# Kernel tuning notes

Measured on AMD Instinct MI355X. Metric: run time of the kernel, lower is better.

## Reference

```python
import jax, jax.numpy as jnp
import numpy as np

C = 512
H = 8
D = C // H
GROUPS = 32
EPS = 1e-5

def setup_inputs() -> dict:
    key = jax.random.key(0)
    ks = jax.random.split(key, 7)
    B, L = 4, 2048
    x = jax.random.normal(ks[0], (B, C, L), dtype=jnp.float32)
    gamma = jnp.ones((C,), dtype=jnp.float32)
    beta = jnp.zeros((C,), dtype=jnp.float32)
    w_qkv = jax.random.normal(ks[1], (3 * C, C), dtype=jnp.float32) * (1.0 / np.sqrt(C))
    b_qkv = jax.random.normal(ks[2], (3 * C,), dtype=jnp.float32) * 0.01
    w_proj = jax.random.normal(ks[3], (C, C), dtype=jnp.float32) * (1.0 / np.sqrt(C))
    b_proj = jax.random.normal(ks[4], (C,), dtype=jnp.float32) * 0.01
    return {"x": x, "gamma": gamma, "beta": beta, "w_qkv": w_qkv,
            "b_qkv": b_qkv, "w_proj": w_proj, "b_proj": b_proj}

def _group_norm(x, gamma, beta):
    B, Cc, L = x.shape
    xg = x.reshape(B, GROUPS, Cc // GROUPS, L)
    mean = jnp.mean(xg, axis=(2, 3), keepdims=True)
    var = jnp.var(xg, axis=(2, 3), keepdims=True)
    xn = ((xg - mean) * jax.lax.rsqrt(var + EPS)).reshape(B, Cc, L)
    return xn * gamma[None, :, None] + beta[None, :, None]

def reference(x, gamma, beta, w_qkv, b_qkv, w_proj, b_proj):
    B, Cc, L = x.shape
    h = _group_norm(x, gamma, beta)
    # 1x1 conv == channel matmul: (3C,C) x (B,C,L) -> (B,3C,L)
    qkv = jnp.einsum('oc,bcl->bol', w_qkv, h) + b_qkv[None, :, None]
    q, k, v = jnp.split(qkv, 3, axis=1)
    # (B,C,L) -> (B,H,L,D)
    def to_heads(t):
        return t.reshape(B, H, D, L).transpose(0, 1, 3, 2)
    q, k, v = to_heads(q), to_heads(k), to_heads(v)
    scale = 1.0 / np.sqrt(D).astype(np.float32)
    attn = jnp.einsum('bhqd,bhkd->bhqk', q, k) * scale  # [B,H,L,L]
    attn = jax.nn.softmax(attn, axis=-1)
    out = jnp.einsum('bhqk,bhkd->bhqd', attn, v)  # [B,H,L,D]
    out = out.transpose(0, 1, 3, 2).reshape(B, Cc, L)
    proj = jnp.einsum('oc,bcl->bol', w_proj, out) + b_proj[None, :, None]
    return x + proj
```

## Files before the change

kernel.cpp:

```cpp
#include <hip/hip_runtime.h>
#include <stdint.h>

#define C_DIM 512
#define H_HEADS 8
#define D_HEAD 64
#define B_BATCH 4
#define L_SEQ 2048
#define GROUPS 32
#define EPS_GN 1e-5f

typedef unsigned short u16;
typedef __attribute__((ext_vector_type(8))) __bf16 bf16x8;
typedef __attribute__((ext_vector_type(2))) float f32x2;
typedef __attribute__((ext_vector_type(4))) float f32x4;
typedef __attribute__((ext_vector_type(16))) float f32x16;

__device__ __forceinline__ u16 f2bf(float f) {
  unsigned u = __builtin_bit_cast(unsigned, f);
  unsigned r = u + 0x7FFFu + ((u >> 16) & 1u);
  return (u16)(r >> 16);
}

__device__ __forceinline__ unsigned cvtpk_bf16(float lo, float hi) {
  unsigned r;
  asm("v_cvt_pk_bf16_f32 %0, %1, %2" : "=v"(r) : "v"(lo), "v"(hi));
  return r;
}

__device__ __forceinline__ void pl32swap(unsigned& a, unsigned& b) {
  asm("v_permlane32_swap_b32 %0, %1" : "+v"(a), "+v"(b));
}

__device__ __forceinline__ bf16x8 mk8(unsigned a, unsigned b, unsigned c, unsigned d) {
  union { uint4 u; bf16x8 v; } z;
  z.u.x = a; z.u.y = b; z.u.z = c; z.u.w = d;
  return z.v;
}

__device__ __forceinline__ void gl16(const void* g, void* l) {
  __builtin_amdgcn_global_load_lds((const __attribute__((address_space(1))) void*)g,
                                   (__attribute__((address_space(3))) void*)l, 16, 0, 0);
}

__global__ __launch_bounds__(256) void prep_kernel(const float* __restrict__ x,
                                                   const float* __restrict__ gamma,
                                                   const float* __restrict__ beta,
                                                   const float* __restrict__ wq,
                                                   const float* __restrict__ wp,
                                                   u16* __restrict__ h_t,
                                                   u16* __restrict__ wq_bf,
                                                   u16* __restrict__ wp_bf) {
  if (blockIdx.x >= 128) {
    int i = (blockIdx.x - 128) * 256 + threadIdx.x;
    const int nq = 3 * C_DIM * C_DIM;
    int idx = i * 4;
    const float* src;
    u16* dst;
    if (idx < nq) { src = wq + idx; dst = wq_bf + idx; }
    else          { src = wp + (idx - nq); dst = wp_bf + (idx - nq); }
    float4 v = *(const float4*)src;
    uint2 pk;
    pk.x = cvtpk_bf16(v.x, v.y);
    pk.y = cvtpk_bf16(v.z, v.w);
    *(uint2*)dst = pk;
    return;
  }
  int bg = blockIdx.x;
  int b = bg >> 5, g = bg & 31;
  const float* base = x + ((size_t)(b * C_DIM + g * 16)) * L_SEQ;
  int t = threadIdx.x;
  int w = t >> 6;
  float s = 0.f, sq = 0.f;
  for (int i = 0; i < 32; ++i) {
    float4 v = ((const float4*)base)[t + i * 256];
    s += v.x + v.y + v.z + v.w;
    sq += v.x * v.x + v.y * v.y + v.z * v.z + v.w * v.w;
  }
  for (int off = 32; off; off >>= 1) { s += __shfl_down(s, off); sq += __shfl_down(sq, off); }
  __shared__ float red[8];
  if ((t & 63) == 0) { red[w * 2] = s; red[w * 2 + 1] = sq; }
  __syncthreads();
  float ts = red[0] + red[2] + red[4] + red[6];
  float tq = red[1] + red[3] + red[5] + red[7];
  float mean = ts * (1.f / 32768.f);
  float var = tq * (1.f / 32768.f) - mean * mean;
  float rstd = rsqrtf(var + EPS_GN);
  float ga[16], be[16];
#pragma unroll
  for (int c = 0; c < 16; ++c) {
    float gm = gamma[g * 16 + c];
    ga[c] = gm * rstd;
    be[c] = beta[g * 16 + c] - mean * gm * rstd;
  }
  __shared__ float tile[16][260];
  for (int lc = 0; lc < 8; ++lc) {
    __syncthreads();
#pragma unroll
    for (int it = 0; it < 4; ++it) {
      int r = it * 4 + w;
      int c4 = (t & 63) * 4;
      *(float4*)&tile[r][c4] = *(const float4*)(base + (size_t)r * L_SEQ + lc * 256 + c4);
    }
    __syncthreads();
    int l = lc * 256 + t;
    unsigned wds[8];
#pragma unroll
    for (int c = 0; c < 8; ++c) {
      float a0 = tile[2 * c][t] * ga[2 * c] + be[2 * c];
      float a1 = tile[2 * c + 1][t] * ga[2 * c + 1] + be[2 * c + 1];
      wds[c] = cvtpk_bf16(a0, a1);
    }
    u16* dst = h_t + ((size_t)(b * L_SEQ + l)) * C_DIM + g * 16;
    uint4 p0; p0.x = wds[0]; p0.y = wds[1]; p0.z = wds[2]; p0.w = wds[3];
    uint4 p1; p1.x = wds[4]; p1.y = wds[5]; p1.z = wds[6]; p1.w = wds[7];
    *(uint4*)dst = p0;
    *(uint4*)(dst + 8) = p1;
  }
}

template <int MODE>
__global__ __launch_bounds__(256) void gemm_kernel(const u16* __restrict__ A_bf,
                                                   const u16* __restrict__ B_t,
                                                   const float* __restrict__ bias,
                                                   const float* __restrict__ xres,
                                                   u16* __restrict__ q_t,
                                                   u16* __restrict__ kf_g,
                                                   u16* __restrict__ vf_g,
                                                   float* __restrict__ out_f) {
  constexpr int K = 512;
  __shared__ u16 A_lds[128][32];
  __shared__ u16 B_lds[128][32];
  int t = threadIdx.x;
  int w = t >> 6, lane = t & 63;
  int q4 = lane >> 4, c15 = lane & 15;
  int wm = w >> 1, wn = w & 1;
  int o0 = blockIdx.y * 128;
  int l0 = blockIdx.x * 128;
  int b = blockIdx.z;
  const u16* Bb = B_t + (size_t)b * L_SEQ * K;
  f32x4 acc[4][4] = {};

  int sr = lane >> 2, sc = lane & 3;
  int r0 = w * 32 + sr;
  int r1 = r0 + 16;
  int lc0 = (sc - (r0 >> 1)) & 3;
  int lc1 = (sc - (r1 >> 1)) & 3;
  const u16* Ag0 = A_bf + (size_t)(o0 + r0) * K + lc0 * 8;
  const u16* Ag1 = A_bf + (size_t)(o0 + r1) * K + lc1 * 8;
  const u16* Bg0 = Bb + (size_t)(l0 + r0) * K + lc0 * 8;
  const u16* Bg1 = Bb + (size_t)(l0 + r1) * K + lc1 * 8;
  u16* Al0 = &A_lds[w * 32][0];
  u16* Al1 = &A_lds[w * 32 + 16][0];
  u16* Bl0 = &B_lds[w * 32][0];
  u16* Bl1 = &B_lds[w * 32 + 16][0];

  for (int kt = 0; kt < K / 32; ++kt) {
    gl16(Ag0, Al0); gl16(Ag1, Al1);
    gl16(Bg0, Bl0); gl16(Bg1, Bl1);
    Ag0 += 32; Ag1 += 32; Bg0 += 32; Bg1 += 32;
    __syncthreads();
    bf16x8 af[4], bfr[4];
#pragma unroll
    for (int mi = 0; mi < 4; ++mi) {
      int ar = wm * 64 + mi * 16 + c15;
      af[mi] = *(const bf16x8*)&A_lds[ar][((q4 + (ar >> 1)) & 3) * 8];
    }
#pragma unroll
    for (int ni = 0; ni < 4; ++ni) {
      int br = wn * 64 + ni * 16 + c15;
      bfr[ni] = *(const bf16x8*)&B_lds[br][((q4 + (br >> 1)) & 3) * 8];
    }
#pragma unroll
    for (int mi = 0; mi < 4; ++mi)
#pragma unroll
      for (int ni = 0; ni < 4; ++ni)
        acc[mi][ni] = __builtin_amdgcn_mfma_f32_16x16x32_bf16(af[mi], bfr[ni], acc[mi][ni], 0, 0, 0);
    __syncthreads();
  }

  if (MODE == 0) {
    const float QS = 0.18033688f;
    int sel = o0 >> 9;
    int ob = o0 - sel * 512 + wm * 64;
#pragma unroll
    for (int mi = 0; mi < 4; ++mi) {
      int orow = ob + mi * 16 + q4 * 4;
      float4 bi = *(const float4*)&bias[o0 + wm * 64 + mi * 16 + q4 * 4];
#pragma unroll
      for (int ni = 0; ni < 4; ++ni) {
        int l = l0 + wn * 64 + ni * 16 + c15;
        float v0 = acc[mi][ni][0] + bi.x;
        float v1 = acc[mi][ni][1] + bi.y;
        float v2 = acc[mi][ni][2] + bi.z;
        float v3 = acc[mi][ni][3] + bi.w;
        if (sel == 0) {
          v0 *= QS; v1 *= QS; v2 *= QS; v3 *= QS;
          uint2 pk;
          pk.x = cvtpk_bf16(v0, v1);
          pk.y = cvtpk_bf16(v2, v3);
          *(uint2*)(q_t + ((size_t)(b * L_SEQ + l)) * C_DIM + orow) = pk;
        } else if (sel == 1) {
          int hh = orow >> 6, d = orow & 63;
          size_t base = ((size_t)(b * 8 + hh)) * 131072 +
                        (size_t)(((l >> 5) * 4 + (d >> 4))) * 512 +
                        (size_t)((l & 31) + ((d >> 3) & 1) * 32) * 8 + (d & 7);
          uint2 pk;
          pk.x = cvtpk_bf16(v0, v1);
          pk.y = cvtpk_bf16(v2, v3);
          *(uint2*)(kf_g + base) = pk;
        } else {
          int hh = orow >> 6, d = orow & 63;
          size_t base0 = ((size_t)(b * 8 + hh)) * 131072 +
                         (size_t)(l >> 4) * 1024 +
                         (size_t)((l >> 3) & 1) * 256 + (l & 7);
          vf_g[base0 + (size_t)((d + 0) >> 5) * 512 + ((d + 0) & 31) * 8] = f2bf(v0);
          vf_g[base0 + (size_t)((d + 1) >> 5) * 512 + ((d + 1) & 31) * 8] = f2bf(v1);
          vf_g[base0 + (size_t)((d + 2) >> 5) * 512 + ((d + 2) & 31) * 8] = f2bf(v2);
          vf_g[base0 + (size_t)((d + 3) >> 5) * 512 + ((d + 3) & 31) * 8] = f2bf(v3);
        }
      }
    }
  } else {
#pragma unroll
    for (int mi = 0; mi < 4; ++mi) {
      int orow = o0 + wm * 64 + mi * 16 + q4 * 4;
      float4 bi = *(const float4*)&bias[orow];
#pragma unroll
      for (int ni = 0; ni < 4; ++ni) {
        int l = l0 + wn * 64 + ni * 16 + c15;
        size_t base2 = ((size_t)(b * C_DIM + orow)) * L_SEQ + l;
        out_f[base2] = acc[mi][ni][0] + bi.x + xres[base2];
        out_f[base2 + L_SEQ] = acc[mi][ni][1] + bi.y + xres[base2 + L_SEQ];
        out_f[base2 + 2 * L_SEQ] = acc[mi][ni][2] + bi.z + xres[base2 + 2 * L_SEQ];
        out_f[base2 + 3 * L_SEQ] = acc[mi][ni][3] + bi.w + xres[base2 + 3 * L_SEQ];
      }
    }
  }
}

#define ATILE(KC, KN, T)                                                       \
  {                                                                            \
    int tn = (T) + 1; tn = tn > 31 ? 31 : tn;                                  \
    const u16* kp = kfb + tn * 2048;                                           \
    const u16* vp = vfb + (T) * 2048;                                          \
    KN[0] = *(const bf16x8*)(kp);                                              \
    KN[1] = *(const bf16x8*)(kp + 512);                                        \
    KN[2] = *(const bf16x8*)(kp + 1024);                                       \
    KN[3] = *(const bf16x8*)(kp + 1536);                                       \
    bf16x8 v0 = *(const bf16x8*)(vp);                                          \
    bf16x8 v1 = *(const bf16x8*)(vp + 512);                                    \
    bf16x8 v2 = *(const bf16x8*)(vp + 1024);                                   \
    bf16x8 v3 = *(const bf16x8*)(vp + 1536);                                   \
    f32x16 s;                                                                  \
    _Pragma("unroll") for (int r = 0; r < 16; ++r) s[r] = 0.f;                 \
    s = __builtin_amdgcn_mfma_f32_32x32x16_bf16(KC[0], qf[0], s, 0, 0, 0);     \
    s = __builtin_amdgcn_mfma_f32_32x32x16_bf16(KC[1], qf[1], s, 0, 0, 0);     \
    s = __builtin_amdgcn_mfma_f32_32x32x16_bf16(KC[2], qf[2], s, 0, 0, 0);     \
    s = __builtin_amdgcn_mfma_f32_32x32x16_bf16(KC[3], qf[3], s, 0, 0, 0);     \
    f32x2 p0_ = {s[0], s[1]}, p1_ = {s[2], s[3]}, p2_ = {s[4], s[5]},          \
          p3_ = {s[6], s[7]}, p4_ = {s[8], s[9]}, p5_ = {s[10], s[11]},        \
          p6_ = {s[12], s[13]}, p7_ = {s[14], s[15]};                          \
    f32x2 M0 = __builtin_elementwise_max(__builtin_elementwise_max(p0_, p1_),  \
                                         __builtin_elementwise_max(p2_, p3_)); \
    f32x2 M1 = __builtin_elementwise_max(__builtin_elementwise_max(p4_, p5_),  \
                                         __builtin_elementwise_max(p6_, p7_)); \
    f32x2 M = __builtin_elementwise_max(M0, M1);                               \
    float mx = fmaxf(M[0], M[1]);                                              \
    mx = fmaxf(mx, __shfl_xor(mx, 32));                                        \
    if (__any(mx > m_r + 8.f)) {                                               \
      float mnew = fmaxf(m_r, mx);                                             \
      float al = __builtin_amdgcn_exp2f(m_r - mnew);                           \
      l_r *= al;                                                               \
      _Pragma("unroll") for (int r = 0; r < 16; ++r) { o0[r] *= al; o1[r] *= al; } \
      m_r = mnew;                                                              \
    }                                                                          \
    _Pragma("unroll") for (int r = 0; r < 16; ++r)                             \
        s[r] = __builtin_amdgcn_exp2f(s[r] - m_r);                             \
    f32x2 a0_ = {s[0], s[1]}, a1_ = {s[2], s[3]}, a2_ = {s[4], s[5]},          \
          a3_ = {s[6], s[7]}, a4_ = {s[8], s[9]}, a5_ = {s[10], s[11]},        \
          a6_ = {s[12], s[13]}, a7_ = {s[14], s[15]};                          \
    f32x2 b0_ = a0_ + a1_, b1_ = a2_ + a3_, b2_ = a4_ + a5_, b3_ = a6_ + a7_;  \
    f32x2 c0_ = b0_ + b1_, c1_ = b2_ + b3_;                                    \
    f32x2 d0_ = c0_ + c1_;                                                     \
    float sum = d0_[0] + d0_[1];                                               \
    sum += __shfl_xor(sum, 32);                                                \
    l_r += sum;                                                                \
    unsigned pk[8];                                                            \
    _Pragma("unroll") for (int i = 0; i < 8; ++i)                              \
        pk[i] = cvtpk_bf16(s[2 * i], s[2 * i + 1]);                            \
    pl32swap(pk[0], pk[2]); pl32swap(pk[1], pk[3]);                            \
    pl32swap(pk[4], pk[6]); pl32swap(pk[5], pk[7]);                            \
    bf16x8 pf0 = mk8(pk[0], pk[1], pk[2], pk[3]);                              \
    bf16x8 pf1 = mk8(pk[4], pk[5], pk[6], pk[7]);                              \
    o0 = __builtin_amdgcn_mfma_f32_32x32x16_bf16(v0, pf0, o0, 0, 0, 0);        \
    o1 = __builtin_amdgcn_mfma_f32_32x32x16_bf16(v1, pf0, o1, 0, 0, 0);        \
    o0 = __builtin_amdgcn_mfma_f32_32x32x16_bf16(v2, pf1, o0, 0, 0, 0);        \
    o1 = __builtin_amdgcn_mfma_f32_32x32x16_bf16(v3, pf1, o1, 0, 0, 0);        \
  }

__global__ __launch_bounds__(256, 4) void attn_kernel(const u16* __restrict__ q_t,
                                                      const u16* __restrict__ kf_g,
                                                      const u16* __restrict__ vf_g,
                                                      u16* __restrict__ ao_t) {
  __shared__ float oL[4][64][32];
  __shared__ float mL[4][32];
  __shared__ float lL[4][32];

  int g = blockIdx.x;
  int wk = (g & 7) * 128 + (g >> 3);
  int qg = wk & 31, bh = wk >> 5;
  int b = bh >> 3, h = bh & 7;
  int t = threadIdx.x;
  int wv = t >> 6, lane = t & 63;
  int q = lane & 31, hi = lane >> 5;
  int qh = wv & 1, kvh = wv >> 1;
  int q0 = qg * 64 + qh * 32;

  const u16* qp = q_t + ((size_t)(b * L_SEQ + q0 + q)) * C_DIM + h * 64 + hi * 8;
  bf16x8 qf[4];
#pragma unroll
  for (int kk = 0; kk < 4; ++kk) qf[kk] = *(const bf16x8*)(qp + kk * 16);

  const u16* kfb = kf_g + (size_t)bh * 131072 + (size_t)kvh * 65536 + lane * 8;
  const u16* vfb = vf_g + (size_t)bh * 131072 + (size_t)kvh * 65536 + lane * 8;

  f32x16 o0, o1;
#pragma unroll
  for (int r = 0; r < 16; ++r) { o0[r] = 0.f; o1[r] = 0.f; }
  float m_r = -1e30f, l_r = 0.f;

  bf16x8 kA[4], kB[4];
#pragma unroll
  for (int i = 0; i < 4; ++i) kA[i] = *(const bf16x8*)(kfb + i * 512);

  for (int it = 0; it < 16; ++it) {
    ATILE(kA, kB, 2 * it);
    ATILE(kB, kA, 2 * it + 1);
  }

  if (hi == 0) mL[wv][q] = m_r;
  __syncthreads();
  float ms = fmaxf(mL[wv][q], mL[wv ^ 2][q]);
  float scl = __builtin_amdgcn_exp2f(m_r - ms);
  if (hi == 0) lL[wv][q] = l_r * scl;
#pragma unroll
  for (int r = 0; r < 16; ++r) {
    int d = (r & 3) + 8 * (r >> 2) + 4 * hi;
    oL[wv][d][q] = o0[r] * scl;
    oL[wv][d + 32][q] = o1[r] * scl;
  }
  __syncthreads();

  int tq = t & 31;
  int oqh = (t >> 5) & 1;
  int d0 = (t >> 6) * 16;
  float lsum = lL[oqh][tq] + lL[oqh + 2][tq];
  float inv = 1.f / lsum;
  float v[16];
#pragma unroll
  for (int i = 0; i < 16; ++i)
    v[i] = (oL[oqh][d0 + i][tq] + oL[oqh + 2][d0 + i][tq]) * inv;
  u16* dst = ao_t + ((size_t)(b * L_SEQ + qg * 64 + oqh * 32 + tq)) * C_DIM + h * 64 + d0;
  uint4 ov0, ov1;
  ov0.x = cvtpk_bf16(v[0], v[1]);
  ov0.y = cvtpk_bf16(v[2], v[3]);
  ov0.z = cvtpk_bf16(v[4], v[5]);
  ov0.w = cvtpk_bf16(v[6], v[7]);
  ov1.x = cvtpk_bf16(v[8], v[9]);
  ov1.y = cvtpk_bf16(v[10], v[11]);
  ov1.z = cvtpk_bf16(v[12], v[13]);
  ov1.w = cvtpk_bf16(v[14], v[15]);
  *(uint4*)dst = ov0;
  *(uint4*)(dst + 8) = ov1;
}

extern "C" void kernel_launch(void* const* d_in, const int* in_sizes, int n_in,
                              void* d_out, int out_size, void* d_ws, size_t ws_size,
                              hipStream_t stream) {
  const float* x = (const float*)d_in[0];
  const float* gamma = (const float*)d_in[1];
  const float* beta = (const float*)d_in[2];
  const float* w_qkv = (const float*)d_in[3];
  const float* b_qkv = (const float*)d_in[4];
  const float* w_proj = (const float*)d_in[5];
  const float* b_proj = (const float*)d_in[6];
  float* out = (float*)d_out;

  u16* wq_bf = (u16*)d_ws;
  u16* wp_bf = wq_bf + 786432;
  u16* h_t = wp_bf + 262144;
  u16* q_t = h_t + 4194304;
  u16* kf_g = q_t + 4194304;
  u16* vf_g = kf_g + 4194304;
  u16* ao_t = vf_g + 4194304;

  prep_kernel<<<dim3(1152), dim3(256), 0, stream>>>(x, gamma, beta, w_qkv, w_proj,
                                                    h_t, wq_bf, wp_bf);
  gemm_kernel<0><<<dim3(16, 12, 4), dim3(256), 0, stream>>>(wq_bf, h_t, b_qkv, nullptr, q_t, kf_g, vf_g, nullptr);
  attn_kernel<<<dim3(1024), dim3(256), 0, stream>>>(q_t, kf_g, vf_g, ao_t);
  gemm_kernel<1><<<dim3(16, 4, 4), dim3(256), 0, stream>>>(wp_bf, ao_t, b_proj, x, nullptr, nullptr, nullptr, out);
}
```

Measured before the change: 105.9 us.

## Compute softmax row sums via MFMA with ones, drop K prefetch, retile proj GEMM

```diff
diff --git a/kernel.cpp b/kernel.cpp
--- a/kernel.cpp
+++ b/kernel.cpp
@@ -118,15 +118,12 @@
   }
 }
 
-template <int MODE>
-__global__ __launch_bounds__(256) void gemm_kernel(const u16* __restrict__ A_bf,
-                                                   const u16* __restrict__ B_t,
-                                                   const float* __restrict__ bias,
-                                                   const float* __restrict__ xres,
-                                                   u16* __restrict__ q_t,
-                                                   u16* __restrict__ kf_g,
-                                                   u16* __restrict__ vf_g,
-                                                   float* __restrict__ out_f) {
+__global__ __launch_bounds__(256) void gemm_qkv(const u16* __restrict__ A_bf,
+                                                const u16* __restrict__ B_t,
+                                                const float* __restrict__ bias,
+                                                u16* __restrict__ q_t,
+                                                u16* __restrict__ kf_g,
+                                                u16* __restrict__ vf_g) {
   constexpr int K = 512;
   __shared__ u16 A_lds[128][32];
   __shared__ u16 B_lds[128][32];
@@ -178,124 +175,176 @@
     __syncthreads();
   }
 
-  if (MODE == 0) {
-    const float QS = 0.18033688f;
-    int sel = o0 >> 9;
-    int ob = o0 - sel * 512 + wm * 64;
+  const float QS = 0.18033688f;
+  int sel = o0 >> 9;
+  int ob = o0 - sel * 512 + wm * 64;
+#pragma unroll
+  for (int mi = 0; mi < 4; ++mi) {
+    int orow = ob + mi * 16 + q4 * 4;
+    float4 bi = *(const float4*)&bias[o0 + wm * 64 + mi * 16 + q4 * 4];
+#pragma unroll
+    for (int ni = 0; ni < 4; ++ni) {
+      int l = l0 + wn * 64 + ni * 16 + c15;
+      float v0 = acc[mi][ni][0] + bi.x;
+      float v1 = acc[mi][ni][1] + bi.y;
+      float v2 = acc[mi][ni][2] + bi.z;
+      float v3 = acc[mi][ni][3] + bi.w;
+      if (sel == 0) {
+        v0 *= QS; v1 *= QS; v2 *= QS; v3 *= QS;
+        uint2 pk;
+        pk.x = cvtpk_bf16(v0, v1);
+        pk.y = cvtpk_bf16(v2, v3);
+        *(uint2*)(q_t + ((size_t)(b * L_SEQ + l)) * C_DIM + orow) = pk;
+      } else if (sel == 1) {
+        int hh = orow >> 6, d = orow & 63;
+        size_t base = ((size_t)(b * 8 + hh)) * 131072 +
+                      (size_t)(((l >> 5) * 4 + (d >> 4))) * 512 +
+                      (size_t)((l & 31) + ((d >> 3) & 1) * 32) * 8 + (d & 7);
+        uint2 pk;
+        pk.x = cvtpk_bf16(v0, v1);
+        pk.y = cvtpk_bf16(v2, v3);
+        *(uint2*)(kf_g + base) = pk;
+      } else {
+        int hh = orow >> 6, d = orow & 63;
+        size_t base0 = ((size_t)(b * 8 + hh)) * 131072 +
+                       (size_t)(l >> 4) * 1024 +
+                       (size_t)((l >> 3) & 1) * 256 + (l & 7);
+        vf_g[base0 + (size_t)((d + 0) >> 5) * 512 + ((d + 0) & 31) * 8] = f2bf(v0);
+        vf_g[base0 + (size_t)((d + 1) >> 5) * 512 + ((d + 1) & 31) * 8] = f2bf(v1);
+        vf_g[base0 + (size_t)((d + 2) >> 5) * 512 + ((d + 2) & 31) * 8] = f2bf(v2);
+        vf_g[base0 + (size_t)((d + 3) >> 5) * 512 + ((d + 3) & 31) * 8] = f2bf(v3);
+      }
+    }
+  }
+}
+
+__global__ __launch_bounds__(256) void gemm_proj(const u16* __restrict__ A_bf,
+                                                 const u16* __restrict__ B_t,
+                                                 const float* __restrict__ bias,
+                                                 const float* __restrict__ xres,
+                                                 float* __restrict__ out_f) {
+  constexpr int K = 512;
+  __shared__ u16 A_lds[64][32];
+  __shared__ u16 B_lds[128][32];
+  int t = threadIdx.x;
+  int w = t >> 6, lane = t & 63;
+  int q4 = lane >> 4, c15 = lane & 15;
+  int o0 = blockIdx.y * 64;
+  int l0 = blockIdx.x * 128;
+  int b = blockIdx.z;
+  const u16* Bb = B_t + (size_t)b * L_SEQ * K;
+  f32x4 acc[4][2] = {};
+
+  int sr = lane >> 2, sc = lane & 3;
+  int ra = w * 16 + sr;
+  int lca = (sc - (ra >> 1)) & 3;
+  const u16* Ag = A_bf + (size_t)(o0 + ra) * K + lca * 8;
+  int rb0 = w * 32 + sr, rb1 = rb0 + 16;
+  int lcb0 = (sc - (rb0 >> 1)) & 3;
+  int lcb1 = (sc - (rb1 >> 1)) & 3;
+  const u16* Bg0 = Bb + (size_t)(l0 + rb0) * K + lcb0 * 8;
+  const u16* Bg1 = Bb + (size_t)(l0 + rb1) * K + lcb1 * 8;
+  u16* Al = &A_lds[w * 16][0];
+  u16* Bl0 = &B_lds[w * 32][0];
+  u16* Bl1 = &B_lds[w * 32 + 16][0];
+
+  for (int kt = 0; kt < K / 32; ++kt) {
+    gl16(Ag, Al);
+    gl16(Bg0, Bl0); gl16(Bg1, Bl1);
+    Ag += 32; Bg0 += 32; Bg1 += 32;
+    __syncthreads();
+    bf16x8 af[4], bfr[2];
 #pragma unroll
     for (int mi = 0; mi < 4; ++mi) {
-      int orow = ob + mi * 16 + q4 * 4;
-      float4 bi = *(const float4*)&bias[o0 + wm * 64 + mi * 16 + q4 * 4];
-#pragma unroll
-      for (int ni = 0; ni < 4; ++ni) {
-        int l = l0 + wn * 64 + ni * 16 + c15;
-        float v0 = acc[mi][ni][0] + bi.x;
-        float v1 = acc[mi][ni][1] + bi.y;
-        float v2 = acc[mi][ni][2] + bi.z;
-        float v3 = acc[mi][ni][3] + bi.w;
-        if (sel == 0) {
-          v0 *= QS; v1 *= QS; v2 *= QS; v3 *= QS;
-          uint2 pk;
-          pk.x = cvtpk_bf16(v0, v1);
-          pk.y = cvtpk_bf16(v2, v3);
-          *(uint2*)(q_t + ((size_t)(b * L_SEQ + l)) * C_DIM + orow) = pk;
-        } else if (sel == 1) {
-          int hh = orow >> 6, d = orow & 63;
-          size_t base = ((size_t)(b * 8 + hh)) * 131072 +
-                        (size_t)(((l >> 5) * 4 + (d >> 4))) * 512 +
-                        (size_t)((l & 31) + ((d >> 3) & 1) * 32) * 8 + (d & 7);
-          uint2 pk;
-          pk.x = cvtpk_bf16(v0, v1);
-          pk.y = cvtpk_bf16(v2, v3);
-          *(uint2*)(kf_g + base) = pk;
-        } else {
-          int hh = orow >> 6, d = orow & 63;
-          size_t base0 = ((size_t)(b * 8 + hh)) * 131072 +
-                         (size_t)(l >> 4) * 1024 +
-                         (size_t)((l >> 3) & 1) * 256 + (l & 7);
-          vf_g[base0 + (size_t)((d + 0) >> 5) * 512 + ((d + 0) & 31) * 8] = f2bf(v0);
-          vf_g[base0 + (size_t)((d + 1) >> 5) * 512 + ((d + 1) & 31) * 8] = f2bf(v1);
-          vf_g[base0 + (size_t)((d + 2) >> 5) * 512 + ((d + 2) & 31) * 8] = f2bf(v2);
-          vf_g[base0 + (size_t)((d + 3) >> 5) * 512 + ((d + 3) & 31) * 8] = f2bf(v3);
-        }
-      }
-    }
-  } else {
-#pragma unroll
-    for (int mi = 0; mi < 4; ++mi) {
-      int orow = o0 + wm * 64 + mi * 16 + q4 * 4;
-      float4 bi = *(const float4*)&bias[orow];
-#pragma unroll
-      for (int ni = 0; ni < 4; ++ni) {
-        int l = l0 + wn * 64 + ni * 16 + c15;
-        size_t base2 = ((size_t)(b * C_DIM + orow)) * L_SEQ + l;
-        out_f[base2] = acc[mi][ni][0] + bi.x + xres[base2];
-        out_f[base2 + L_SEQ] = acc[mi][ni][1] + bi.y + xres[base2 + L_SEQ];
-        out_f[base2 + 2 * L_SEQ] = acc[mi][ni][2] + bi.z + xres[base2 + 2 * L_SEQ];
-        out_f[base2 + 3 * L_SEQ] = acc[mi][ni][3] + bi.w + xres[base2 + 3 * L_SEQ];
-      }
-    }
-  }
-}
-
-#define ATILE(KC, KN, T)                                                       \
+      int ar = mi * 16 + c15;
+      af[mi] = *(const bf16x8*)&A_lds[ar][((q4 + (ar >> 1)) & 3) * 8];
+    }
+#pragma unroll
+    for (int ni = 0; ni < 2; ++ni) {
+      int br = w * 32 + ni * 16 + c15;
+      bfr[ni] = *(const bf16x8*)&B_lds[br][((q4 + (br >> 1)) & 3) * 8];
+    }
+#pragma unroll
+    for (int mi = 0; mi < 4; ++mi)
+#pragma unroll
+      for (int ni = 0; ni < 2; ++ni)
+        acc[mi][ni] = __builtin_amdgcn_mfma_f32_16x16x32_bf16(af[mi], bfr[ni], acc[mi][ni], 0, 0, 0);
+    __syncthreads();
+  }
+
+#pragma unroll
+  for (int mi = 0; mi < 4; ++mi) {
+    int orow = o0 + mi * 16 + q4 * 4;
+    float4 bi = *(const float4*)&bias[orow];
+#pragma unroll
+    for (int ni = 0; ni < 2; ++ni) {
+      int l = l0 + w * 32 + ni * 16 + c15;
+      size_t base2 = ((size_t)(b * C_DIM + orow)) * L_SEQ + l;
+      out_f[base2] = acc[mi][ni][0] + bi.x + xres[base2];
+      out_f[base2 + L_SEQ] = acc[mi][ni][1] + bi.y + xres[base2 + L_SEQ];
+      out_f[base2 + 2 * L_SEQ] = acc[mi][ni][2] + bi.z + xres[base2 + 2 * L_SEQ];
+      out_f[base2 + 3 * L_SEQ] = acc[mi][ni][3] + bi.w + xres[base2 + 3 * L_SEQ];
+    }
+  }
+}
+
+#define ATILE(T)                                                               \
   {                                                                            \
-    int tn = (T) + 1; tn = tn > 31 ? 31 : tn;                                  \
-    const u16* kp = kfb + tn * 2048;                                           \
+    const u16* kp = kfb + (T) * 2048;                                          \
     const u16* vp = vfb + (T) * 2048;                                          \
-    KN[0] = *(const bf16x8*)(kp);                                              \
-    KN[1] = *(const bf16x8*)(kp + 512);                                        \
-    KN[2] = *(const bf16x8*)(kp + 1024);                                       \
-    KN[3] = *(const bf16x8*)(kp + 1536);                                       \
+    bf16x8 k0 = *(const bf16x8*)(kp);                                          \
+    bf16x8 k1 = *(const bf16x8*)(kp + 512);                                    \
+    bf16x8 k2 = *(const bf16x8*)(kp + 1024);                                   \
+    bf16x8 k3 = *(const bf16x8*)(kp + 1536);                                   \
+    f32x16 s;                                                                  \
+    _Pragma("unroll") for (int r = 0; r < 16; ++r) s[r] = 0.f;                 \
+    s = __builtin_amdgcn_mfma_f32_32x32x16_bf16(k0, qf[0], s, 0, 0, 0);        \
+    s = __builtin_amdgcn_mfma_f32_32x32x16_bf16(k1, qf[1], s, 0, 0, 0);        \
+    s = __builtin_amdgcn_mfma_f32_32x32x16_bf16(k2, qf[2], s, 0, 0, 0);        \
+    s = __builtin_amdgcn_mfma_f32_32x32x16_bf16(k3, qf[3], s, 0, 0, 0);        \
     bf16x8 v0 = *(const bf16x8*)(vp);                                          \
     bf16x8 v1 = *(const bf16x8*)(vp + 512);                                    \
     bf16x8 v2 = *(const bf16x8*)(vp + 1024);                                   \
     bf16x8 v3 = *(const bf16x8*)(vp + 1536);                                   \
-    f32x16 s;                                                                  \
-    _Pragma("unroll") for (int r = 0; r < 16; ++r) s[r] = 0.f;                 \
-    s = __builtin_amdgcn_mfma_f32_32x32x16_bf16(KC[0], qf[0], s, 0, 0, 0);     \
-    s = __builtin_amdgcn_mfma_f32_32x32x16_bf16(KC[1], qf[1], s, 0, 0, 0);     \
-    s = __builtin_amdgcn_mfma_f32_32x32x16_bf16(KC[2], qf[2], s, 0, 0, 0);     \
-    s = __builtin_amdgcn_mfma_f32_32x32x16_bf16(KC[3], qf[3], s, 0, 0, 0);     \
-    f32x2 p0_ = {s[0], s[1]}, p1_ = {s[2], s[3]}, p2_ = {s[4], s[5]},          \
-          p3_ = {s[6], s[7]}, p4_ = {s[8], s[9]}, p5_ = {s[10], s[11]},        \
-          p6_ = {s[12], s[13]}, p7_ = {s[14], s[15]};                          \
-    f32x2 M0 = __builtin_elementwise_max(__builtin_elementwise_max(p0_, p1_),  \
-                                         __builtin_elementwise_max(p2_, p3_)); \
-    f32x2 M1 = __builtin_elementwise_max(__builtin_elementwise_max(p4_, p5_),  \
-                                         __builtin_elementwise_max(p6_, p7_)); \
+    f32x2 e0 = {s[0], s[1]}, e1 = {s[2], s[3]}, e2 = {s[4], s[5]},             \
+          e3 = {s[6], s[7]}, e4 = {s[8], s[9]}, e5 = {s[10], s[11]},           \
+          e6 = {s[12], s[13]}, e7 = {s[14], s[15]};                            \
+    f32x2 M0 = __builtin_elementwise_max(__builtin_elementwise_max(e0, e1),    \
+                                         __builtin_elementwise_max(e2, e3));   \
+    f32x2 M1 = __builtin_elementwise_max(__builtin_elementwise_max(e4, e5),    \
+                                         __builtin_elementwise_max(e6, e7));   \
     f32x2 M = __builtin_elementwise_max(M0, M1);                               \
     float mx = fmaxf(M[0], M[1]);                                              \
     mx = fmaxf(mx, __shfl_xor(mx, 32));                                        \
     if (__any(mx > m_r + 8.f)) {                                               \
       float mnew = fmaxf(m_r, mx);                                             \
       float al = __builtin_amdgcn_exp2f(m_r - mnew);                           \
-      l_r *= al;                                                               \
-      _Pragma("unroll") for (int r = 0; r < 16; ++r) { o0[r] *= al; o1[r] *= al; } \
+      lacc[0] *= al;                                                           \
+      _Pragma("unroll") for (int r = 0; r < 16; ++r) { o0a[r] *= al; o1a[r] *= al; } \
       m_r = mnew;                                                              \
     }                                                                          \
-    _Pragma("unroll") for (int r = 0; r < 16; ++r)                             \
-        s[r] = __builtin_amdgcn_exp2f(s[r] - m_r);                             \
-    f32x2 a0_ = {s[0], s[1]}, a1_ = {s[2], s[3]}, a2_ = {s[4], s[5]},          \
-          a3_ = {s[6], s[7]}, a4_ = {s[8], s[9]}, a5_ = {s[10], s[11]},        \
-          a6_ = {s[12], s[13]}, a7_ = {s[14], s[15]};                          \
-    f32x2 b0_ = a0_ + a1_, b1_ = a2_ + a3_, b2_ = a4_ + a5_, b3_ = a6_ + a7_;  \
-    f32x2 c0_ = b0_ + b1_, c1_ = b2_ + b3_;                                    \
-    f32x2 d0_ = c0_ + c1_;                                                     \
-    float sum = d0_[0] + d0_[1];                                               \
-    sum += __shfl_xor(sum, 32);                                                \
-    l_r += sum;                                                                \
+    f32x2 nm = {-m_r, -m_r};                                                   \
+    e0 += nm; e1 += nm; e2 += nm; e3 += nm;                                    \
+    e4 += nm; e5 += nm; e6 += nm; e7 += nm;                                    \
     unsigned pk[8];                                                            \
-    _Pragma("unroll") for (int i = 0; i < 8; ++i)                              \
-        pk[i] = cvtpk_bf16(s[2 * i], s[2 * i + 1]);                            \
+    pk[0] = cvtpk_bf16(__builtin_amdgcn_exp2f(e0[0]), __builtin_amdgcn_exp2f(e0[1])); \
+    pk[1] = cvtpk_bf16(__builtin_amdgcn_exp2f(e1[0]), __builtin_amdgcn_exp2f(e1[1])); \
+    pk[2] = cvtpk_bf16(__builtin_amdgcn_exp2f(e2[0]), __builtin_amdgcn_exp2f(e2[1])); \
+    pk[3] = cvtpk_bf16(__builtin_amdgcn_exp2f(e3[0]), __builtin_amdgcn_exp2f(e3[1])); \
+    pk[4] = cvtpk_bf16(__builtin_amdgcn_exp2f(e4[0]), __builtin_amdgcn_exp2f(e4[1])); \
+    pk[5] = cvtpk_bf16(__builtin_amdgcn_exp2f(e5[0]), __builtin_amdgcn_exp2f(e5[1])); \
+    pk[6] = cvtpk_bf16(__builtin_amdgcn_exp2f(e6[0]), __builtin_amdgcn_exp2f(e6[1])); \
+    pk[7] = cvtpk_bf16(__builtin_amdgcn_exp2f(e7[0]), __builtin_amdgcn_exp2f(e7[1])); \
     pl32swap(pk[0], pk[2]); pl32swap(pk[1], pk[3]);                            \
     pl32swap(pk[4], pk[6]); pl32swap(pk[5], pk[7]);                            \
     bf16x8 pf0 = mk8(pk[0], pk[1], pk[2], pk[3]);                              \
     bf16x8 pf1 = mk8(pk[4], pk[5], pk[6], pk[7]);                              \
-    o0 = __builtin_amdgcn_mfma_f32_32x32x16_bf16(v0, pf0, o0, 0, 0, 0);        \
-    o1 = __builtin_amdgcn_mfma_f32_32x32x16_bf16(v1, pf0, o1, 0, 0, 0);        \
-    o0 = __builtin_amdgcn_mfma_f32_32x32x16_bf16(v2, pf1, o0, 0, 0, 0);        \
-    o1 = __builtin_amdgcn_mfma_f32_32x32x16_bf16(v3, pf1, o1, 0, 0, 0);        \
+    lacc = __builtin_amdgcn_mfma_f32_32x32x16_bf16(ones, pf0, lacc, 0, 0, 0);  \
+    lacc = __builtin_amdgcn_mfma_f32_32x32x16_bf16(ones, pf1, lacc, 0, 0, 0);  \
+    o0a = __builtin_amdgcn_mfma_f32_32x32x16_bf16(v0, pf0, o0a, 0, 0, 0);      \
+    o1a = __builtin_amdgcn_mfma_f32_32x32x16_bf16(v1, pf0, o1a, 0, 0, 0);      \
+    o0a = __builtin_amdgcn_mfma_f32_32x32x16_bf16(v2, pf1, o0a, 0, 0, 0);      \
+    o1a = __builtin_amdgcn_mfma_f32_32x32x16_bf16(v3, pf1, o1a, 0, 0, 0);      \
   }
 
 __global__ __launch_bounds__(256, 4) void attn_kernel(const u16* __restrict__ q_t,
@@ -324,30 +373,27 @@
   const u16* kfb = kf_g + (size_t)bh * 131072 + (size_t)kvh * 65536 + lane * 8;
   const u16* vfb = vf_g + (size_t)bh * 131072 + (size_t)kvh * 65536 + lane * 8;
 
-  f32x16 o0, o1;
-#pragma unroll
-  for (int r = 0; r < 16; ++r) { o0[r] = 0.f; o1[r] = 0.f; }
-  float m_r = -1e30f, l_r = 0.f;
-
-  bf16x8 kA[4], kB[4];
-#pragma unroll
-  for (int i = 0; i < 4; ++i) kA[i] = *(const bf16x8*)(kfb + i * 512);
-
-  for (int it = 0; it < 16; ++it) {
-    ATILE(kA, kB, 2 * it);
-    ATILE(kB, kA, 2 * it + 1);
+  const bf16x8 ones = mk8(0x3F803F80u, 0x3F803F80u, 0x3F803F80u, 0x3F803F80u);
+
+  f32x16 o0a, o1a, lacc;
+#pragma unroll
+  for (int r = 0; r < 16; ++r) { o0a[r] = 0.f; o1a[r] = 0.f; lacc[r] = 0.f; }
+  float m_r = -1e30f;
+
+  for (int it = 0; it < 32; ++it) {
+    ATILE(it);
   }
 
   if (hi == 0) mL[wv][q] = m_r;
   __syncthreads();
   float ms = fmaxf(mL[wv][q], mL[wv ^ 2][q]);
   float scl = __builtin_amdgcn_exp2f(m_r - ms);
-  if (hi == 0) lL[wv][q] = l_r * scl;
+  if (hi == 0) lL[wv][q] = lacc[0] * scl;
 #pragma unroll
   for (int r = 0; r < 16; ++r) {
     int d = (r & 3) + 8 * (r >> 2) + 4 * hi;
-    oL[wv][d][q] = o0[r] * scl;
-    oL[wv][d + 32][q] = o1[r] * scl;
+    oL[wv][d][q] = o0a[r] * scl;
+    oL[wv][d + 32][q] = o1a[r] * scl;
   }
   __syncthreads();
 
@@ -396,7 +442,7 @@
 
   prep_kernel<<<dim3(1152), dim3(256), 0, stream>>>(x, gamma, beta, w_qkv, w_proj,
                                                     h_t, wq_bf, wp_bf);
-  gemm_kernel<0><<<dim3(16, 12, 4), dim3(256), 0, stream>>>(wq_bf, h_t, b_qkv, nullptr, q_t, kf_g, vf_g, nullptr);
+  gemm_qkv<<<dim3(16, 12, 4), dim3(256), 0, stream>>>(wq_bf, h_t, b_qkv, q_t, kf_g, vf_g);
   attn_kernel<<<dim3(1024), dim3(256), 0, stream>>>(q_t, kf_g, vf_g, ao_t);
-  gemm_kernel<1><<<dim3(16, 4, 4), dim3(256), 0, stream>>>(wp_bf, ao_t, b_proj, x, nullptr, nullptr, nullptr, out);
-}
+  gemm_proj<<<dim3(16, 8, 4), dim3(256), 0, stream>>>(wp_bf, ao_t, b_proj, x, out);
+}
```

After: 107.0 us. No clear change (+0.9%).
